# Optimization experiments

Hardware: AMD Instinct MI355X
Metric: run time of the kernel (lower is better)

## Reference

```python
import jax, jax.numpy as jnp
import numpy as np

K = 512
D = 256


def setup_inputs() -> dict:
    key = jax.random.key(0)
    k1, k2 = jax.random.split(key)
    x = jax.random.normal(k1, (64, D, 32, 32), dtype=jnp.float32)
    # nn.Embedding(K, D) init: uniform(-1/K, 1/K)
    emb = jax.random.uniform(k2, (K, D), dtype=jnp.float32, minval=-1.0 / K, maxval=1.0 / K)
    return {"x": x, "emb": emb}


def reference(x, emb):
    # encoder is identity: z_e_x = x, shape [B, D, H, W]
    B, Dd, H, W = x.shape
    z_e = jnp.transpose(x, (0, 2, 3, 1))           # [B, H, W, D]
    z_flat = z_e.reshape(-1, Dd)                    # [N, D]
    # squared euclidean distances to codebook: ||z||^2 + ||e||^2 - 2 z.e
    dist = (jnp.sum(z_flat * z_flat, axis=1, keepdims=True)
            + jnp.sum(emb * emb, axis=1)[None, :]
            - 2.0 * z_flat @ emb.T)                 # [N, K]
    idx = jnp.argmin(dist, axis=1)                  # [N]
    codes = emb[idx]                                # [N, D] gather
    codes = codes.reshape(B, H, W, Dd)
    # straight-through quantized output (value == codes)
    z_q_st = z_e + jax.lax.stop_gradient(codes - z_e)
    z_q_st = jnp.transpose(z_q_st, (0, 3, 1, 2))    # [B, D, H, W]
    # z_q_x_bar: gathered from live codebook (grads flow to emb)
    z_q_bar = jnp.transpose(codes, (0, 3, 1, 2))    # [B, D, H, W]
    # decoder is identity: x_tilde = z_q_st
    return (z_q_st, x, z_q_bar)
```

## Files before the change

kernel.cpp:

```cpp
#include <hip/hip_runtime.h>


#define B_  64
#define D_  256
#define HW_ 1024
#define K_  512

typedef __attribute__((ext_vector_type(8))) short short8;
typedef __attribute__((ext_vector_type(4))) float f32x4;

__device__ unsigned short g_ebf[K_ * D_];
__device__ float g_e2[K_];

__device__ __forceinline__ unsigned short f2bf(float f) {
    unsigned u = __float_as_uint(f);
    u += 0x7fffu + ((u >> 16) & 1u);
    return (unsigned short)(u >> 16);
}

__global__ void prep(const float* __restrict__ emb) {
    const int t   = threadIdx.x;
    const int row = blockIdx.x * 8 + (t >> 5);
    const int c0  = (t & 31) * 8;
    const float* rp = emb + row * D_ + c0;
    float4 a = *(const float4*)rp;
    float4 b = *(const float4*)(rp + 4);
    short8 v;
    v[0] = (short)f2bf(a.x); v[1] = (short)f2bf(a.y);
    v[2] = (short)f2bf(a.z); v[3] = (short)f2bf(a.w);
    v[4] = (short)f2bf(b.x); v[5] = (short)f2bf(b.y);
    v[6] = (short)f2bf(b.z); v[7] = (short)f2bf(b.w);
    *(short8*)(g_ebf + row * D_ + c0) = v;
    float ps = a.x*a.x + a.y*a.y + a.z*a.z + a.w*a.w
             + b.x*b.x + b.y*b.y + b.z*b.z + b.w*b.w;
    ps += __shfl_xor(ps, 1);  ps += __shfl_xor(ps, 2);
    ps += __shfl_xor(ps, 4);  ps += __shfl_xor(ps, 8);
    ps += __shfl_xor(ps, 16);
    if ((t & 31) == 0) g_e2[row] = ps;
}

__global__ __launch_bounds__(256, 2)
void vq_main(const float* __restrict__ x, const float* __restrict__ emb,
             float* __restrict__ out0, float* __restrict__ out1,
             float* __restrict__ out2) {
    __shared__ float zc[4][32][36];
    __shared__ int   idxs[128];

    const int t   = threadIdx.x;
    const int w   = t >> 6;
    const int l   = t & 63;
    const int blk = blockIdx.x;
    const int b   = blk >> 3;
    const int hw0 = (blk & 7) << 7;
    const float* xb = x    + ((size_t)b * D_) * HW_ + hw0;
    float*       o1 = out1 + ((size_t)b * D_) * HW_ + hw0;
    const int hwb = w * 32;

    short8 zb[2][8];
    for (int g = 0; g < 8; ++g) {
#pragma unroll
        for (int it = 0; it < 4; ++it) {
            const int d2 = 8 * it + (l >> 3);
            const int dr = 32 * g + d2;
            const int cc = (l & 7) * 4;
            float4 v = *(const float4*)&xb[(size_t)dr * HW_ + hwb + cc];
            *(float4*)&o1[(size_t)dr * HW_ + hwb + cc] = v;
            *(float4*)&zc[w][d2][cc] = v;
        }
        __syncthreads();
#pragma unroll
        for (int t2 = 0; t2 < 2; ++t2) {
            const int p = 16 * t2 + (l & 15);
            short8 f;
#pragma unroll
            for (int j = 0; j < 8; ++j)
                f[j] = (short)f2bf(zc[w][(l >> 4) * 8 + j][p]);
            zb[t2][g] = f;
        }
        __syncthreads();
    }

    float minv0 = 3.0e38f, minv1 = 3.0e38f;
    int   mini0 = 0,       mini1 = 0;
    short8 ea[8], eb[8];
    f32x4  e2a, e2b;

#define LOADE(buf, e2r, ct) do {                                              \
        const unsigned short* _p = g_ebf + ((ct) * 16 + (l & 15)) * D_        \
                                   + (l >> 4) * 8;                            \
        _Pragma("unroll")                                                     \
        for (int s = 0; s < 8; ++s) buf[s] = *(const short8*)(_p + s * 32);   \
        e2r = *(const f32x4*)(g_e2 + (ct) * 16 + (l >> 4) * 4);               \
    } while (0)

#define PROC(buf, e2v, ct) do {                                               \
        f32x4 a0 = {0.f, 0.f, 0.f, 0.f}, a1 = {0.f, 0.f, 0.f, 0.f};          \
        _Pragma("unroll")                                                     \
        for (int s = 0; s < 8; ++s) {                                         \
            a0 = __builtin_amdgcn_mfma_f32_16x16x32_bf16(buf[s], zb[0][s], a0, 0, 0, 0); \
            a1 = __builtin_amdgcn_mfma_f32_16x16x32_bf16(buf[s], zb[1][s], a1, 0, 0, 0); \
        }                                                                     \
        _Pragma("unroll")                                                     \
        for (int r = 0; r < 4; ++r) {                                         \
            const int code = (ct) * 16 + (l >> 4) * 4 + r;                    \
            const float s0 = e2v[r] - 2.0f * a0[r];                           \
            const float s1 = e2v[r] - 2.0f * a1[r];                           \
            if (s0 < minv0) { minv0 = s0; mini0 = code; }                     \
            if (s1 < minv1) { minv1 = s1; mini1 = code; }                     \
        }                                                                     \
    } while (0)

    LOADE(ea, e2a, 0);
    for (int c = 0; c < 32; c += 2) {
        LOADE(eb, e2b, c + 1);
        PROC(ea, e2a, c);
        const int cn = (c + 2 < 32) ? (c + 2) : 0;
        LOADE(ea, e2a, cn);
        PROC(eb, e2b, c + 1);
    }

    {
        float ov; int oi;
        ov = __shfl_xor(minv0, 16); oi = __shfl_xor(mini0, 16);
        if (ov < minv0 || (ov == minv0 && oi < mini0)) { minv0 = ov; mini0 = oi; }
        ov = __shfl_xor(minv0, 32); oi = __shfl_xor(mini0, 32);
        if (ov < minv0 || (ov == minv0 && oi < mini0)) { minv0 = ov; mini0 = oi; }
        ov = __shfl_xor(minv1, 16); oi = __shfl_xor(mini1, 16);
        if (ov < minv1 || (ov == minv1 && oi < mini1)) { minv1 = ov; mini1 = oi; }
        ov = __shfl_xor(minv1, 32); oi = __shfl_xor(mini1, 32);
        if (ov < minv1 || (ov == minv1 && oi < mini1)) { minv1 = ov; mini1 = oi; }
    }
    if ((l >> 4) == 0) {
        idxs[w * 32 + (l & 15)]      = mini0;
        idxs[w * 32 + 16 + (l & 15)] = mini1;
    }
    __syncthreads();

    {
        const int n  = t & 127;
        const int dg = t >> 7;
        const float* erow = emb + (size_t)idxs[n] * D_;
        float* p0 = out0 + ((size_t)b * D_) * HW_ + hw0 + n;
        float* p2 = out2 + ((size_t)b * D_) * HW_ + hw0 + n;
#pragma unroll 4
        for (int i = 0; i < 32; ++i) {
            const int d = dg * 4 + i * 8;
            float4 v = *(const float4*)&erow[d];
            p0[(size_t)(d + 0) * HW_] = v.x; p0[(size_t)(d + 1) * HW_] = v.y;
            p0[(size_t)(d + 2) * HW_] = v.z; p0[(size_t)(d + 3) * HW_] = v.w;
            p2[(size_t)(d + 0) * HW_] = v.x; p2[(size_t)(d + 1) * HW_] = v.y;
            p2[(size_t)(d + 2) * HW_] = v.z; p2[(size_t)(d + 3) * HW_] = v.w;
        }
    }
}

extern "C" void kernel_launch(void* const* d_in, const int* in_sizes, int n_in,
                              void* d_out, int out_size, void* d_ws, size_t ws_size,
                              hipStream_t stream) {
    const float* x   = (const float*)d_in[0];
    const float* emb = (const float*)d_in[1];
    float* out0 = (float*)d_out;
    float* out1 = out0 + (size_t)16777216;
    float* out2 = out0 + (size_t)33554432;

    prep<<<64, 256, 0, stream>>>(emb);
    vq_main<<<512, 256, 0, stream>>>(x, emb, out0, out1, out2);
}
```

Before: 305.3 us.

## Halve per-block tile, double-buffer x staging, add nontemporal stores

Each block now covers 64 spatial positions instead of 128, so the grid doubles to 1024 blocks and launch bounds allow 4 blocks per CU. Each wave handles 16 positions with one accumulator. The x tile load into shared memory is double-buffered so the next 32-channel slab loads while the current one is converted to bf16. The argmin index stays in registers, which drops the shared idxs array and a barrier. All output writes use nontemporal stores to reduce cache pollution from the large streaming outputs. The trade-off is that every block re-reads the full bf16 codebook, so codebook traffic doubles.

```diff
diff --git a/kernel.cpp b/kernel.cpp
--- a/kernel.cpp
+++ b/kernel.cpp
@@ -1,7 +1,6 @@
 #include <hip/hip_runtime.h>
 
 
-#define B_  64
 #define D_  256
 #define HW_ 1024
 #define K_  512
@@ -39,74 +38,83 @@
     if ((t & 31) == 0) g_e2[row] = ps;
 }
 
-__global__ __launch_bounds__(256, 2)
+__global__ __launch_bounds__(256, 4)
 void vq_main(const float* __restrict__ x, const float* __restrict__ emb,
              float* __restrict__ out0, float* __restrict__ out1,
              float* __restrict__ out2) {
-    __shared__ float zc[4][32][36];
-    __shared__ int   idxs[128];
+    __shared__ float zc[2][32][68];
 
     const int t   = threadIdx.x;
     const int w   = t >> 6;
     const int l   = t & 63;
+    const int lq  = l >> 4;
+    const int lp  = l & 15;
     const int blk = blockIdx.x;
-    const int b   = blk >> 3;
-    const int hw0 = (blk & 7) << 7;
+    const int b   = blk >> 4;
+    const int hw0 = (blk & 15) << 6;
     const float* xb = x    + ((size_t)b * D_) * HW_ + hw0;
     float*       o1 = out1 + ((size_t)b * D_) * HW_ + hw0;
-    const int hwb = w * 32;
 
-    short8 zb[2][8];
+    const int d2a = (t >> 4);
+    const int q4  = (t & 15) << 2;
+
+    {
+#pragma unroll
+        for (int it = 0; it < 2; ++it) {
+            const int d2 = it * 16 + d2a;
+            f32x4 v = *(const f32x4*)&xb[(size_t)d2 * HW_ + q4];
+            __builtin_nontemporal_store(v, (f32x4*)&o1[(size_t)d2 * HW_ + q4]);
+            *(f32x4*)&zc[0][d2][q4] = v;
+        }
+    }
+    __syncthreads();
+
+    short8 zb[8];
     for (int g = 0; g < 8; ++g) {
-#pragma unroll
-        for (int it = 0; it < 4; ++it) {
-            const int d2 = 8 * it + (l >> 3);
-            const int dr = 32 * g + d2;
-            const int cc = (l & 7) * 4;
-            float4 v = *(const float4*)&xb[(size_t)dr * HW_ + hwb + cc];
-            *(float4*)&o1[(size_t)dr * HW_ + hwb + cc] = v;
-            *(float4*)&zc[w][d2][cc] = v;
+        f32x4 v0, v1;
+        if (g < 7) {
+            const int dr = 32 * (g + 1);
+            v0 = *(const f32x4*)&xb[(size_t)(dr + d2a) * HW_ + q4];
+            v1 = *(const f32x4*)&xb[(size_t)(dr + 16 + d2a) * HW_ + q4];
+            __builtin_nontemporal_store(v0, (f32x4*)&o1[(size_t)(dr + d2a) * HW_ + q4]);
+            __builtin_nontemporal_store(v1, (f32x4*)&o1[(size_t)(dr + 16 + d2a) * HW_ + q4]);
         }
-        __syncthreads();
-#pragma unroll
-        for (int t2 = 0; t2 < 2; ++t2) {
-            const int p = 16 * t2 + (l & 15);
+        {
             short8 f;
 #pragma unroll
             for (int j = 0; j < 8; ++j)
-                f[j] = (short)f2bf(zc[w][(l >> 4) * 8 + j][p]);
-            zb[t2][g] = f;
+                f[j] = (short)f2bf(zc[g & 1][lq * 8 + j][16 * w + lp]);
+            zb[g] = f;
+        }
+        if (g < 7) {
+            *(f32x4*)&zc[(g + 1) & 1][d2a][q4]      = v0;
+            *(f32x4*)&zc[(g + 1) & 1][16 + d2a][q4] = v1;
         }
         __syncthreads();
     }
 
-    float minv0 = 3.0e38f, minv1 = 3.0e38f;
-    int   mini0 = 0,       mini1 = 0;
+    float minv = 3.0e38f;
+    int   mini = 0;
     short8 ea[8], eb[8];
     f32x4  e2a, e2b;
 
 #define LOADE(buf, e2r, ct) do {                                              \
-        const unsigned short* _p = g_ebf + ((ct) * 16 + (l & 15)) * D_        \
-                                   + (l >> 4) * 8;                            \
+        const unsigned short* _p = g_ebf + ((ct) * 16 + lp) * D_ + lq * 8;    \
         _Pragma("unroll")                                                     \
         for (int s = 0; s < 8; ++s) buf[s] = *(const short8*)(_p + s * 32);   \
-        e2r = *(const f32x4*)(g_e2 + (ct) * 16 + (l >> 4) * 4);               \
+        e2r = *(const f32x4*)(g_e2 + (ct) * 16 + lq * 4);                     \
     } while (0)
 
 #define PROC(buf, e2v, ct) do {                                               \
-        f32x4 a0 = {0.f, 0.f, 0.f, 0.f}, a1 = {0.f, 0.f, 0.f, 0.f};          \
+        f32x4 a0 = {0.f, 0.f, 0.f, 0.f};                                      \
         _Pragma("unroll")                                                     \
-        for (int s = 0; s < 8; ++s) {                                         \
-            a0 = __builtin_amdgcn_mfma_f32_16x16x32_bf16(buf[s], zb[0][s], a0, 0, 0, 0); \
-            a1 = __builtin_amdgcn_mfma_f32_16x16x32_bf16(buf[s], zb[1][s], a1, 0, 0, 0); \
-        }                                                                     \
+        for (int s = 0; s < 8; ++s)                                           \
+            a0 = __builtin_amdgcn_mfma_f32_16x16x32_bf16(buf[s], zb[s], a0, 0, 0, 0); \
         _Pragma("unroll")                                                     \
         for (int r = 0; r < 4; ++r) {                                         \
-            const int code = (ct) * 16 + (l >> 4) * 4 + r;                    \
+            const int code = (ct) * 16 + lq * 4 + r;                          \
             const float s0 = e2v[r] - 2.0f * a0[r];                           \
-            const float s1 = e2v[r] - 2.0f * a1[r];                           \
-            if (s0 < minv0) { minv0 = s0; mini0 = code; }                     \
-            if (s1 < minv1) { minv1 = s1; mini1 = code; }                     \
+            if (s0 < minv) { minv = s0; mini = code; }                        \
         }                                                                     \
     } while (0)
 
@@ -121,35 +129,28 @@
 
     {
         float ov; int oi;
-        ov = __shfl_xor(minv0, 16); oi = __shfl_xor(mini0, 16);
-        if (ov < minv0 || (ov == minv0 && oi < mini0)) { minv0 = ov; mini0 = oi; }
-        ov = __shfl_xor(minv0, 32); oi = __shfl_xor(mini0, 32);
-        if (ov < minv0 || (ov == minv0 && oi < mini0)) { minv0 = ov; mini0 = oi; }
-        ov = __shfl_xor(minv1, 16); oi = __shfl_xor(mini1, 16);
-        if (ov < minv1 || (ov == minv1 && oi < mini1)) { minv1 = ov; mini1 = oi; }
-        ov = __shfl_xor(minv1, 32); oi = __shfl_xor(mini1, 32);
-        if (ov < minv1 || (ov == minv1 && oi < mini1)) { minv1 = ov; mini1 = oi; }
+        ov = __shfl_xor(minv, 16); oi = __shfl_xor(mini, 16);
+        if (ov < minv || (ov == minv && oi < mini)) { minv = ov; mini = oi; }
+        ov = __shfl_xor(minv, 32); oi = __shfl_xor(mini, 32);
+        if (ov < minv || (ov == minv && oi < mini)) { minv = ov; mini = oi; }
     }
-    if ((l >> 4) == 0) {
-        idxs[w * 32 + (l & 15)]      = mini0;
-        idxs[w * 32 + 16 + (l & 15)] = mini1;
-    }
-    __syncthreads();
 
     {
-        const int n  = t & 127;
-        const int dg = t >> 7;
-        const float* erow = emb + (size_t)idxs[n] * D_;
-        float* p0 = out0 + ((size_t)b * D_) * HW_ + hw0 + n;
-        float* p2 = out2 + ((size_t)b * D_) * HW_ + hw0 + n;
+        const float* erow = emb + (size_t)mini * D_;
+        float* p0 = out0 + ((size_t)b * D_) * HW_ + hw0 + 16 * w + lp;
+        float* p2 = out2 + ((size_t)b * D_) * HW_ + hw0 + 16 * w + lp;
 #pragma unroll 4
-        for (int i = 0; i < 32; ++i) {
-            const int d = dg * 4 + i * 8;
-            float4 v = *(const float4*)&erow[d];
-            p0[(size_t)(d + 0) * HW_] = v.x; p0[(size_t)(d + 1) * HW_] = v.y;
-            p0[(size_t)(d + 2) * HW_] = v.z; p0[(size_t)(d + 3) * HW_] = v.w;
-            p2[(size_t)(d + 0) * HW_] = v.x; p2[(size_t)(d + 1) * HW_] = v.y;
-            p2[(size_t)(d + 2) * HW_] = v.z; p2[(size_t)(d + 3) * HW_] = v.w;
+        for (int i = 0; i < 16; ++i) {
+            const int d = lq * 4 + i * 16;
+            f32x4 v = *(const f32x4*)&erow[d];
+            __builtin_nontemporal_store(v.x, &p0[(size_t)(d + 0) * HW_]);
+            __builtin_nontemporal_store(v.y, &p0[(size_t)(d + 1) * HW_]);
+            __builtin_nontemporal_store(v.z, &p0[(size_t)(d + 2) * HW_]);
+            __builtin_nontemporal_store(v.w, &p0[(size_t)(d + 3) * HW_]);
+            __builtin_nontemporal_store(v.x, &p2[(size_t)(d + 0) * HW_]);
+            __builtin_nontemporal_store(v.y, &p2[(size_t)(d + 1) * HW_]);
+            __builtin_nontemporal_store(v.z, &p2[(size_t)(d + 2) * HW_]);
+            __builtin_nontemporal_store(v.w, &p2[(size_t)(d + 3) * HW_]);
         }
     }
 }
@@ -164,5 +165,5 @@
     float* out2 = out0 + (size_t)33554432;
 
     prep<<<64, 256, 0, stream>>>(emb);
-    vq_main<<<512, 256, 0, stream>>>(x, emb, out0, out1, out2);
+    vq_main<<<1024, 256, 0, stream>>>(x, emb, out0, out1, out2);
 }
```

Result: slower. 369.5 us (+21.0%).
